# Optimization experiments

Hardware: AMD Instinct MI355X
Metric: run time of the kernel (lower is better)

Reference implementation:

```python
import jax, jax.numpy as jnp
import numpy as np

N = 50000
E = 800000
IN_DIM = 128
OUT_DIM = 128
EDGE_DIM = 3
H = 4
HD = OUT_DIM // H  # 32
SCALE = HD ** -0.5


def setup_inputs() -> dict:
    key = jax.random.key(0)
    ks = jax.random.split(key, 10)
    x = jax.random.normal(ks[0], (N, IN_DIM), dtype=jnp.float32)
    edge_index = jax.random.randint(ks[1], (2, E), 0, N, dtype=jnp.int64)
    edge_attr = jax.random.normal(ks[2], (E, EDGE_DIM), dtype=jnp.float32)
    s = 1.0 / np.sqrt(IN_DIM)
    Wq = jax.random.normal(ks[3], (IN_DIM, H * HD), dtype=jnp.float32) * s
    Wk = jax.random.normal(ks[4], (IN_DIM, H * HD), dtype=jnp.float32) * s
    Wv = jax.random.normal(ks[5], (IN_DIM, H * HD), dtype=jnp.float32) * s
    We = jax.random.normal(ks[6], (EDGE_DIM, H), dtype=jnp.float32) * (1.0 / np.sqrt(EDGE_DIM))
    Wo = jax.random.normal(ks[7], (H * HD, OUT_DIM), dtype=jnp.float32) * (1.0 / np.sqrt(H * HD))
    bo = jnp.zeros((OUT_DIM,), dtype=jnp.float32)
    Wm = jax.random.normal(ks[8], (IN_DIM + OUT_DIM, OUT_DIM), dtype=jnp.float32) * (1.0 / np.sqrt(IN_DIM + OUT_DIM))
    bm = jnp.zeros((OUT_DIM,), dtype=jnp.float32)
    return {"x": x, "edge_index": edge_index, "edge_attr": edge_attr,
            "Wq": Wq, "Wk": Wk, "Wv": Wv, "We": We, "Wo": Wo, "bo": bo,
            "Wm": Wm, "bm": bm}


def reference(x, edge_index, edge_attr, Wq, Wk, Wv, We, Wo, bo, Wm, bm):
    n = x.shape[0]
    src = edge_index[0]
    dst = edge_index[1]
    Q = (x @ Wq).reshape(n, H, HD)
    K = (x @ Wk).reshape(n, H, HD)
    V = (x @ Wv).reshape(n, H, HD)
    edge_bias = edge_attr @ We                                  # [E, H]
    attn = jnp.sum(Q[dst] * K[src], axis=-1) * SCALE + edge_bias  # [E, H]
    attn = jnp.where(attn >= 0, attn, 0.2 * attn)               # leaky_relu(0.2)
    # NOTE: original uses a single GLOBAL max over all edges/heads for stability
    attn_exp = jnp.exp(attn - jnp.max(attn))
    attn_sum = jax.ops.segment_sum(attn_exp, dst, num_segments=n)  # [N, H]
    attn_norm = attn_exp / jnp.maximum(attn_sum[dst], 1e-12)
    # dropout disabled (eval mode)
    weighted_V = V[src] * attn_norm[:, :, None]                 # [E, H, HD]
    agg = jax.ops.segment_sum(weighted_V, dst, num_segments=n)  # [N, H, HD]
    agg = agg.reshape(n, H * HD) @ Wo + bo                      # [N, OUT]
    h = jnp.concatenate([x, agg], axis=1) @ Wm + bm
    return jax.nn.relu(h)
```

## Files before the change

kernel.cpp:

```cpp
#include <hip/hip_runtime.h>
#include <hip/hip_bf16.h>
#include <math.h>

#define NN 50000
#define NE 800000
#define DIM 128
#define NH 4
#define HD 32
#define EH (NE * NH)
#define ATTN_SCALE 0.17677669529663687f
#define MTILE 64
#define GEMM_BLOCKS 782
#define NBKT 98
#define PTS 2048
#define PBLKS 391
#define HBLKS 104

typedef unsigned int uint;
typedef unsigned short ushort;
typedef __attribute__((ext_vector_type(8))) short short8;
typedef __attribute__((ext_vector_type(4))) float f32x4;

__device__ inline ushort f2bf(float f) {
    __hip_bfloat16 h = __float2bfloat16(f);
    return *(ushort*)&h;
}
__device__ inline float bflo(uint u) { return __uint_as_float(u << 16); }
__device__ inline float bfhi(uint u) { return __uint_as_float(u & 0xffff0000u); }

__global__ __launch_bounds__(256) void prep_x_kernel(
    const float* __restrict__ x, ushort* __restrict__ xb)
{
    const int i = blockIdx.x * 256 + threadIdx.x;
    const float4 v = ((const float4*)x)[i];
    ushort4 o;
    o.x = f2bf(v.x); o.y = f2bf(v.y); o.z = f2bf(v.z); o.w = f2bf(v.w);
    ((ushort4*)xb)[i] = o;
}

__global__ __launch_bounds__(128) void prep_wx_kernel(
    const float* __restrict__ Wo, const float* __restrict__ Wm,
    float* __restrict__ Wx)
{
    const int r = blockIdx.x, j = threadIdx.x;
    float acc = 0.f;
    for (int t = 0; t < 128; ++t)
        acc = fmaf(Wo[r * 128 + t], Wm[(128 + t) * 128 + j], acc);
    Wx[r * 128 + j] = acc;
}

__global__ __launch_bounds__(128) void prep_bias_kernel(
    const float* __restrict__ bo, const float* __restrict__ bm,
    const float* __restrict__ Wm, float* __restrict__ bprime)
{
    const int j = threadIdx.x;
    float acc = bm[j];
    for (int t = 0; t < 128; ++t)
        acc = fmaf(bo[t], Wm[(128 + t) * 128 + j], acc);
    bprime[j] = acc;
}

__global__ __launch_bounds__(256) void pack_qkv_kernel(
    const float* __restrict__ Wq, const float* __restrict__ Wk,
    const float* __restrict__ Wv, short* __restrict__ Bp)
{
    const int idx = blockIdx.x * 256 + threadIdx.x;
    const int j = idx & 7, lane = (idx >> 3) & 63;
    const int rest = idx >> 9;
    const int nt = rest % 24, kc = rest / 24;
    const int k = kc * 32 + (lane >> 4) * 8 + j;
    const int n = nt * 16 + (lane & 15);
    const float* W = (n < 128) ? Wq : (n < 256 ? Wk : Wv);
    Bp[idx] = (short)f2bf(W[k * 128 + (n & 127)]);
}

__global__ __launch_bounds__(256) void pack_out_kernel(
    const float* __restrict__ Wm, const float* __restrict__ Wx,
    short* __restrict__ Bp)
{
    const int idx = blockIdx.x * 256 + threadIdx.x;
    const int j = idx & 7, lane = (idx >> 3) & 63;
    const int rest = idx >> 9;
    const int nt = rest & 7, kc = rest >> 3;
    const int k = kc * 32 + (lane >> 4) * 8 + j;
    const int n = nt * 16 + (lane & 15);
    const float v = (k < 128) ? Wm[k * 128 + n] : Wx[(k - 128) * 128 + n];
    Bp[idx] = (short)f2bf(v);
}

__global__ __launch_bounds__(128) void bkt_zero_kernel(int* __restrict__ bkt_cnt)
{
    if (threadIdx.x < 128) bkt_cnt[threadIdx.x] = 0;
}

__global__ __launch_bounds__(256) void bkt_hist_kernel(
    const int* __restrict__ dst, int* __restrict__ bkt_cnt)
{
    __shared__ int c[NBKT];
    const int tid = threadIdx.x;
    if (tid < NBKT) c[tid] = 0;
    __syncthreads();
    for (int e = blockIdx.x * 256 + tid; e < NE; e += HBLKS * 256)
        atomicAdd(&c[dst[e] >> 9], 1);
    __syncthreads();
    if (tid < NBKT && c[tid]) atomicAdd(&bkt_cnt[tid], c[tid]);
}

__global__ void bkt_scan_kernel(const int* __restrict__ bkt_cnt,
                                int* __restrict__ bkt_base,
                                int* __restrict__ bkt_cursor,
                                int* __restrict__ rowptr)
{
    if (threadIdx.x == 0) {
        int run = 0;
        for (int b = 0; b < NBKT; ++b) {
            bkt_base[b] = run;
            bkt_cursor[b] = run;
            run += bkt_cnt[b];
        }
        bkt_base[NBKT] = run;
        rowptr[NN] = run;
    }
}

__global__ __launch_bounds__(256) void partition_kernel(
    const int* __restrict__ src, const int* __restrict__ dst,
    const float* __restrict__ edge_attr, const float* __restrict__ We,
    int* __restrict__ bkt_cursor,
    int* __restrict__ psrc, int* __restrict__ pdst, float* __restrict__ peb)
{
    __shared__ int cnt[NBKT], rbase[NBKT], cnt2[NBKT];
    const int tid = threadIdx.x;
    if (tid < NBKT) cnt[tid] = 0;
    __syncthreads();
    const int e0 = blockIdx.x * PTS;
    #pragma unroll
    for (int it = 0; it < 8; ++it) {
        const int e = e0 + it * 256 + tid;
        if (e < NE) atomicAdd(&cnt[dst[e] >> 9], 1);
    }
    __syncthreads();
    if (tid < NBKT) {
        rbase[tid] = cnt[tid] ? atomicAdd(&bkt_cursor[tid], cnt[tid]) : 0;
        cnt2[tid] = 0;
    }
    __syncthreads();
    #pragma unroll
    for (int it = 0; it < 8; ++it) {
        const int e = e0 + it * 256 + tid;
        if (e < NE) {
            const int d = dst[e];
            const int b = d >> 9;
            const int r = atomicAdd(&cnt2[b], 1);
            const int pos = rbase[b] + r;
            psrc[pos] = src[e];
            pdst[pos] = d;
            const float a0 = edge_attr[e * 3 + 0];
            const float a1 = edge_attr[e * 3 + 1];
            const float a2 = edge_attr[e * 3 + 2];
            float4 eb;
            eb.x = a0 * We[0] + a1 * We[4] + a2 * We[8];
            eb.y = a0 * We[1] + a1 * We[5] + a2 * We[9];
            eb.z = a0 * We[2] + a1 * We[6] + a2 * We[10];
            eb.w = a0 * We[3] + a1 * We[7] + a2 * We[11];
            *(float4*)(peb + (size_t)pos * 4) = eb;
        }
    }
}

__global__ __launch_bounds__(256) void bucket_csr_kernel(
    const int* __restrict__ bkt_base,
    const int* __restrict__ psrc, const int* __restrict__ pdst,
    const float* __restrict__ peb,
    int* __restrict__ rowptr,
    int* __restrict__ srcp, float* __restrict__ eb_csr)
{
    __shared__ int cnt[512];
    __shared__ int pre[512];
    __shared__ int sc[256];
    const int tid = threadIdx.x;
    const int b = blockIdx.x;
    const int base = bkt_base[b];
    const int n = bkt_base[b + 1] - base;
    const int node0 = b << 9;

    cnt[tid] = 0; cnt[tid + 256] = 0;
    __syncthreads();
    for (int i = base + tid; i < base + n; i += 256)
        atomicAdd(&cnt[pdst[i] - node0], 1);
    __syncthreads();

    const int pair = cnt[2 * tid] + cnt[2 * tid + 1];
    sc[tid] = pair;
    __syncthreads();
    for (int off = 1; off < 256; off <<= 1) {
        const int v = (tid >= off) ? sc[tid - off] : 0;
        __syncthreads();
        sc[tid] += v;
        __syncthreads();
    }
    const int ex = sc[tid] - pair;
    pre[2 * tid] = base + ex;
    pre[2 * tid + 1] = base + ex + cnt[2 * tid];
    __syncthreads();

    for (int l = tid; l < 512; l += 256) {
        const int g = node0 + l;
        if (g < NN) rowptr[g] = pre[l];
    }
    __syncthreads();

    for (int i = base + tid; i < base + n; i += 256) {
        const int d = pdst[i];
        const int pos = atomicAdd(&pre[d - node0], 1);
        srcp[pos] = psrc[i];
        *(float4*)(eb_csr + (size_t)pos * 4) =
            *(const float4*)(peb + (size_t)i * 4);
    }
}

__global__ __launch_bounds__(256) void qkv_mfma_kernel(
    const ushort* __restrict__ xb, const short* __restrict__ Bp,
    ushort* __restrict__ Qb, ushort* __restrict__ Kb, ushort* __restrict__ Vb)
{
    const int wave = threadIdx.x >> 6;
    const int lane = threadIdx.x & 63;
    const int m = lane & 15, quad = lane >> 4;
    const int row0w = blockIdx.x * MTILE + wave * 16;
    const int arow = row0w + m;
    const bool rowok = arow < NN;

    short8 a[4];
    #pragma unroll
    for (int kc = 0; kc < 4; ++kc)
        a[kc] = rowok ? *(const short8*)(xb + (size_t)arow * 128 + kc * 32 + quad * 8)
                      : (short8)(0);

    const int NT = 24;
    for (int nt = 0; nt < NT; nt += 2) {
        f32x4 acc0 = {0.f, 0.f, 0.f, 0.f}, acc1 = {0.f, 0.f, 0.f, 0.f};
        #pragma unroll
        for (int kc = 0; kc < 4; ++kc) {
            const short8 b0 = *(const short8*)(Bp + ((size_t)(kc * NT + nt) * 64 + lane) * 8);
            const short8 b1 = *(const short8*)(Bp + ((size_t)(kc * NT + nt + 1) * 64 + lane) * 8);
            acc0 = __builtin_amdgcn_mfma_f32_16x16x32_bf16(a[kc], b0, acc0, 0, 0, 0);
            acc1 = __builtin_amdgcn_mfma_f32_16x16x32_bf16(a[kc], b1, acc1, 0, 0, 0);
        }
        #pragma unroll
        for (int t = 0; t < 2; ++t) {
            const f32x4 acc = t ? acc1 : acc0;
            const int c = (nt + t) * 16 + m;
            ushort* dstp_ = (c < 128) ? Qb : (c < 256 ? Kb : Vb);
            const int lc = c & 127;
            #pragma unroll
            for (int g = 0; g < 4; ++g) {
                const int r = row0w + quad * 4 + g;
                if (r < NN) dstp_[(size_t)r * 128 + lc] = f2bf(acc[g]);
            }
        }
    }
}

__global__ __launch_bounds__(256) void out_mfma_kernel(
    const ushort* __restrict__ xb, const ushort* __restrict__ aggb,
    const short* __restrict__ Bp, const float* __restrict__ bprime,
    float* __restrict__ out)
{
    const int wave = threadIdx.x >> 6;
    const int lane = threadIdx.x & 63;
    const int m = lane & 15, quad = lane >> 4;
    const int row0w = blockIdx.x * MTILE + wave * 16;
    const int arow = row0w + m;
    const bool rowok = arow < NN;

    short8 a[8];
    #pragma unroll
    for (int kc = 0; kc < 4; ++kc)
        a[kc] = rowok ? *(const short8*)(xb + (size_t)arow * 128 + kc * 32 + quad * 8)
                      : (short8)(0);
    #pragma unroll
    for (int kc = 0; kc < 4; ++kc)
        a[4 + kc] = rowok ? *(const short8*)(aggb + (size_t)arow * 128 + kc * 32 + quad * 8)
                          : (short8)(0);

    const int NT = 8;
    for (int nt = 0; nt < NT; nt += 2) {
        f32x4 acc0 = {0.f, 0.f, 0.f, 0.f}, acc1 = {0.f, 0.f, 0.f, 0.f};
        #pragma unroll
        for (int kc = 0; kc < 8; ++kc) {
            const short8 b0 = *(const short8*)(Bp + ((size_t)(kc * NT + nt) * 64 + lane) * 8);
            const short8 b1 = *(const short8*)(Bp + ((size_t)(kc * NT + nt + 1) * 64 + lane) * 8);
            acc0 = __builtin_amdgcn_mfma_f32_16x16x32_bf16(a[kc], b0, acc0, 0, 0, 0);
            acc1 = __builtin_amdgcn_mfma_f32_16x16x32_bf16(a[kc], b1, acc1, 0, 0, 0);
        }
        #pragma unroll
        for (int t = 0; t < 2; ++t) {
            const f32x4 acc = t ? acc1 : acc0;
            const int c = (nt + t) * 16 + m;
            const float bb = bprime[c];
            #pragma unroll
            for (int g = 0; g < 4; ++g) {
                const int r = row0w + quad * 4 + g;
                if (r < NN) out[(size_t)r * 128 + c] = fmaxf(acc[g] + bb, 0.f);
            }
        }
    }
}

__global__ __launch_bounds__(256) void attn_agg_kernel(
    const ushort* __restrict__ Qb, const ushort* __restrict__ Kb,
    const ushort* __restrict__ Vb,
    const int* __restrict__ rowptr, const int* __restrict__ srcp,
    const float* __restrict__ eb_csr, ushort* __restrict__ aggb)
{
    const int tid = threadIdx.x;
    const int d = blockIdx.x * 4 + (tid >> 6);
    const int jj = tid & 63;
    const int h = jj >> 4;
    const int begin = rowptr[d];
    const int end   = rowptr[d + 1];

    const uint uq = *(const uint*)(Qb + (size_t)d * DIM + 2 * jj);
    const float q0 = bflo(uq), q1 = bfhi(uq);

    float ss0 = 0.f, ss1 = 0.f, ss2 = 0.f, ss3 = 0.f;
    float x0 = 0.f, x1 = 0.f, x2 = 0.f, x3 = 0.f;
    float y0 = 0.f, y1 = 0.f, y2 = 0.f, y3 = 0.f;

    int p = begin;
    for (; p + 4 <= end; p += 4) {
        const int s0 = srcp[p + 0];
        const int s1 = srcp[p + 1];
        const int s2 = srcp[p + 2];
        const int s3 = srcp[p + 3];
        const uint k0 = *(const uint*)(Kb + (size_t)s0 * DIM + 2 * jj);
        const uint k1 = *(const uint*)(Kb + (size_t)s1 * DIM + 2 * jj);
        const uint k2 = *(const uint*)(Kb + (size_t)s2 * DIM + 2 * jj);
        const uint k3 = *(const uint*)(Kb + (size_t)s3 * DIM + 2 * jj);
        float p0 = fmaf(q0, bflo(k0), q1 * bfhi(k0));
        float p1 = fmaf(q0, bflo(k1), q1 * bfhi(k1));
        float p2 = fmaf(q0, bflo(k2), q1 * bfhi(k2));
        float p3 = fmaf(q0, bflo(k3), q1 * bfhi(k3));
        #pragma unroll
        for (int m2 = 1; m2 <= 8; m2 <<= 1) {
            p0 += __shfl_xor(p0, m2);
            p1 += __shfl_xor(p1, m2);
            p2 += __shfl_xor(p2, m2);
            p3 += __shfl_xor(p3, m2);
        }
        float a0 = fmaf(p0, ATTN_SCALE, eb_csr[(size_t)(p + 0) * 4 + h]);
        float a1 = fmaf(p1, ATTN_SCALE, eb_csr[(size_t)(p + 1) * 4 + h]);
        float a2 = fmaf(p2, ATTN_SCALE, eb_csr[(size_t)(p + 2) * 4 + h]);
        float a3 = fmaf(p3, ATTN_SCALE, eb_csr[(size_t)(p + 3) * 4 + h]);
        a0 = (a0 >= 0.f) ? a0 : 0.2f * a0;
        a1 = (a1 >= 0.f) ? a1 : 0.2f * a1;
        a2 = (a2 >= 0.f) ? a2 : 0.2f * a2;
        a3 = (a3 >= 0.f) ? a3 : 0.2f * a3;
        const float w0 = __expf(a0);
        const float w1 = __expf(a1);
        const float w2 = __expf(a2);
        const float w3 = __expf(a3);
        const uint v0 = *(const uint*)(Vb + (size_t)s0 * DIM + 2 * jj);
        const uint v1 = *(const uint*)(Vb + (size_t)s1 * DIM + 2 * jj);
        const uint v2 = *(const uint*)(Vb + (size_t)s2 * DIM + 2 * jj);
        const uint v3 = *(const uint*)(Vb + (size_t)s3 * DIM + 2 * jj);
        ss0 += w0; ss1 += w1; ss2 += w2; ss3 += w3;
        x0 = fmaf(w0, bflo(v0), x0); y0 = fmaf(w0, bfhi(v0), y0);
        x1 = fmaf(w1, bflo(v1), x1); y1 = fmaf(w1, bfhi(v1), y1);
        x2 = fmaf(w2, bflo(v2), x2); y2 = fmaf(w2, bfhi(v2), y2);
        x3 = fmaf(w3, bflo(v3), x3); y3 = fmaf(w3, bfhi(v3), y3);
    }
    for (; p < end; ++p) {
        const int s = srcp[p];
        const uint uk = *(const uint*)(Kb + (size_t)s * DIM + 2 * jj);
        float part = fmaf(q0, bflo(uk), q1 * bfhi(uk));
        part += __shfl_xor(part, 1);
        part += __shfl_xor(part, 2);
        part += __shfl_xor(part, 4);
        part += __shfl_xor(part, 8);
        float a = fmaf(part, ATTN_SCALE, eb_csr[(size_t)p * 4 + h]);
        a = (a >= 0.f) ? a : 0.2f * a;
        const float w = __expf(a);
        const uint uv = *(const uint*)(Vb + (size_t)s * DIM + 2 * jj);
        ss0 += w;
        x0 = fmaf(w, bflo(uv), x0);
        y0 = fmaf(w, bfhi(uv), y0);
    }
    const float ssum = (ss0 + ss1) + (ss2 + ss3);
    const float inv = 1.f / fmaxf(ssum, 1e-12f);
    const float ax = ((x0 + x1) + (x2 + x3)) * inv;
    const float ay = ((y0 + y1) + (y2 + y3)) * inv;
    const uint packed = (uint)f2bf(ax) | ((uint)f2bf(ay) << 16);
    *(uint*)(aggb + (size_t)d * DIM + 2 * jj) = packed;
}

extern "C" void kernel_launch(void* const* d_in, const int* in_sizes, int n_in,
                              void* d_out, int out_size, void* d_ws, size_t ws_size,
                              hipStream_t stream)
{
    const float* x         = (const float*)d_in[0];
    const int*   edge_idx  = (const int*)d_in[1];
    const float* edge_attr = (const float*)d_in[2];
    const float* Wq        = (const float*)d_in[3];
    const float* Wk        = (const float*)d_in[4];
    const float* Wv        = (const float*)d_in[5];
    const float* We        = (const float*)d_in[6];
    const float* Wo        = (const float*)d_in[7];
    const float* bo        = (const float*)d_in[8];
    const float* Wm        = (const float*)d_in[9];
    const float* bm        = (const float*)d_in[10];
    float* out = (float*)d_out;

    const int* src = edge_idx;
    const int* dst = edge_idx + NE;

    ushort* xb   = (ushort*)d_ws;
    ushort* Qb   = xb + (size_t)NN * DIM;
    ushort* Kb   = Qb + (size_t)NN * DIM;
    ushort* Vb   = Kb + (size_t)NN * DIM;
    ushort* aggb = Vb + (size_t)NN * DIM;
    int*   psrc     = (int*)(aggb + (size_t)NN * DIM);
    int*   pdst     = psrc + NE;
    float* peb      = (float*)(pdst + NE);
    float* eb_csr   = peb + (size_t)EH;
    float* Wx       = eb_csr + (size_t)EH;
    float* bprime   = Wx + 16384;
    short* BpQKV    = (short*)(bprime + 128);
    short* BpOut    = BpQKV + 49152;
    int*   rowptr   = (int*)(BpOut + 32768);
    int*   srcp     = rowptr + 50048;
    int*   bkt_cnt    = srcp + NE;
    int*   bkt_base   = bkt_cnt + 128;
    int*   bkt_cursor = bkt_base + 128;

    prep_x_kernel<<<(NN * DIM / 4) / 256, 256, 0, stream>>>(x, xb);
    prep_wx_kernel<<<128, 128, 0, stream>>>(Wo, Wm, Wx);
    prep_bias_kernel<<<1, 128, 0, stream>>>(bo, bm, Wm, bprime);
    pack_qkv_kernel<<<192, 256, 0, stream>>>(Wq, Wk, Wv, BpQKV);
    pack_out_kernel<<<128, 256, 0, stream>>>(Wm, Wx, BpOut);

    bkt_zero_kernel<<<1, 128, 0, stream>>>(bkt_cnt);
    bkt_hist_kernel<<<HBLKS, 256, 0, stream>>>(dst, bkt_cnt);
    bkt_scan_kernel<<<1, 64, 0, stream>>>(bkt_cnt, bkt_base, bkt_cursor, rowptr);
    partition_kernel<<<PBLKS, 256, 0, stream>>>(src, dst, edge_attr, We,
                                                bkt_cursor, psrc, pdst, peb);
    bucket_csr_kernel<<<NBKT, 256, 0, stream>>>(bkt_base, psrc, pdst, peb,
                                                rowptr, srcp, eb_csr);

    qkv_mfma_kernel<<<GEMM_BLOCKS, 256, 0, stream>>>(xb, BpQKV, Qb, Kb, Vb);
    attn_agg_kernel<<<NN / 4, 256, 0, stream>>>(Qb, Kb, Vb, rowptr, srcp,
                                                eb_csr, aggb);
    out_mfma_kernel<<<GEMM_BLOCKS, 256, 0, stream>>>(xb, aggb, BpOut, bprime, out);
}
```

Baseline: 295.9 us.

## Interleave K and V rows, store edge bias as bf16, pre-scale src offsets

K and V are written into one interleaved buffer of 256 bf16 per node, so each gathered source node's K and V sit in the same contiguous 512-byte span. This is meant to improve cache and DRAM locality for the random gathers in the attention kernel. Edge bias is packed to bf16 (8 bytes per edge instead of 16), which cuts traffic in partition, CSR build and attention, at some cost in precision. Source indices are stored pre-shifted by 8 so the gather offset needs no multiply, which limits node count to what fits in an int after the shift.

After: 297.0 us. About the same (+0.4%).

```diff
diff --git a/kernel.cpp b/kernel.cpp
--- a/kernel.cpp
+++ b/kernel.cpp
@@ -27,6 +27,7 @@
 }
 __device__ inline float bflo(uint u) { return __uint_as_float(u << 16); }
 __device__ inline float bfhi(uint u) { return __uint_as_float(u & 0xffff0000u); }
+__device__ inline float bfus(ushort u) { return __uint_as_float(((uint)u) << 16); }
 
 __global__ __launch_bounds__(256) void prep_x_kernel(
     const float* __restrict__ x, ushort* __restrict__ xb)
@@ -127,7 +128,7 @@
     const int* __restrict__ src, const int* __restrict__ dst,
     const float* __restrict__ edge_attr, const float* __restrict__ We,
     int* __restrict__ bkt_cursor,
-    int* __restrict__ psrc, int* __restrict__ pdst, float* __restrict__ peb)
+    int* __restrict__ psrc, int* __restrict__ pdst, uint2* __restrict__ peb)
 {
     __shared__ int cnt[NBKT], rbase[NBKT], cnt2[NBKT];
     const int tid = threadIdx.x;
@@ -158,12 +159,14 @@
             const float a0 = edge_attr[e * 3 + 0];
             const float a1 = edge_attr[e * 3 + 1];
             const float a2 = edge_attr[e * 3 + 2];
-            float4 eb;
-            eb.x = a0 * We[0] + a1 * We[4] + a2 * We[8];
-            eb.y = a0 * We[1] + a1 * We[5] + a2 * We[9];
-            eb.z = a0 * We[2] + a1 * We[6] + a2 * We[10];
-            eb.w = a0 * We[3] + a1 * We[7] + a2 * We[11];
-            *(float4*)(peb + (size_t)pos * 4) = eb;
+            const float ex = a0 * We[0] + a1 * We[4] + a2 * We[8];
+            const float ey = a0 * We[1] + a1 * We[5] + a2 * We[9];
+            const float ez = a0 * We[2] + a1 * We[6] + a2 * We[10];
+            const float ew = a0 * We[3] + a1 * We[7] + a2 * We[11];
+            uint2 pk;
+            pk.x = (uint)f2bf(ex) | ((uint)f2bf(ey) << 16);
+            pk.y = (uint)f2bf(ez) | ((uint)f2bf(ew) << 16);
+            peb[pos] = pk;
         }
     }
 }
@@ -171,9 +174,9 @@
 __global__ __launch_bounds__(256) void bucket_csr_kernel(
     const int* __restrict__ bkt_base,
     const int* __restrict__ psrc, const int* __restrict__ pdst,
-    const float* __restrict__ peb,
+    const uint2* __restrict__ peb,
     int* __restrict__ rowptr,
-    int* __restrict__ srcp, float* __restrict__ eb_csr)
+    int* __restrict__ srcp, uint2* __restrict__ eb_csr)
 {
     __shared__ int cnt[512];
     __shared__ int pre[512];
@@ -213,15 +216,14 @@
     for (int i = base + tid; i < base + n; i += 256) {
         const int d = pdst[i];
         const int pos = atomicAdd(&pre[d - node0], 1);
-        srcp[pos] = psrc[i];
-        *(float4*)(eb_csr + (size_t)pos * 4) =
-            *(const float4*)(peb + (size_t)i * 4);
+        srcp[pos] = psrc[i] << 8;
+        eb_csr[pos] = peb[i];
     }
 }
 
 __global__ __launch_bounds__(256) void qkv_mfma_kernel(
     const ushort* __restrict__ xb, const short* __restrict__ Bp,
-    ushort* __restrict__ Qb, ushort* __restrict__ Kb, ushort* __restrict__ Vb)
+    ushort* __restrict__ Qb, ushort* __restrict__ KVb)
 {
     const int wave = threadIdx.x >> 6;
     const int lane = threadIdx.x & 63;
@@ -250,12 +252,13 @@
         for (int t = 0; t < 2; ++t) {
             const f32x4 acc = t ? acc1 : acc0;
             const int c = (nt + t) * 16 + m;
-            ushort* dstp_ = (c < 128) ? Qb : (c < 256 ? Kb : Vb);
-            const int lc = c & 127;
             #pragma unroll
             for (int g = 0; g < 4; ++g) {
                 const int r = row0w + quad * 4 + g;
-                if (r < NN) dstp_[(size_t)r * 128 + lc] = f2bf(acc[g]);
+                if (r < NN) {
+                    if (c < 128) Qb[(size_t)r * 128 + c] = f2bf(acc[g]);
+                    else         KVb[(size_t)r * 256 + (c - 128)] = f2bf(acc[g]);
+                }
             }
         }
     }
@@ -308,10 +311,9 @@
 }
 
 __global__ __launch_bounds__(256) void attn_agg_kernel(
-    const ushort* __restrict__ Qb, const ushort* __restrict__ Kb,
-    const ushort* __restrict__ Vb,
+    const ushort* __restrict__ Qb, const ushort* __restrict__ KVb,
     const int* __restrict__ rowptr, const int* __restrict__ srcp,
-    const float* __restrict__ eb_csr, ushort* __restrict__ aggb)
+    const ushort* __restrict__ ebh, ushort* __restrict__ aggb)
 {
     const int tid = threadIdx.x;
     const int d = blockIdx.x * 4 + (tid >> 6);
@@ -329,14 +331,14 @@
 
     int p = begin;
     for (; p + 4 <= end; p += 4) {
-        const int s0 = srcp[p + 0];
-        const int s1 = srcp[p + 1];
-        const int s2 = srcp[p + 2];
-        const int s3 = srcp[p + 3];
-        const uint k0 = *(const uint*)(Kb + (size_t)s0 * DIM + 2 * jj);
-        const uint k1 = *(const uint*)(Kb + (size_t)s1 * DIM + 2 * jj);
-        const uint k2 = *(const uint*)(Kb + (size_t)s2 * DIM + 2 * jj);
-        const uint k3 = *(const uint*)(Kb + (size_t)s3 * DIM + 2 * jj);
+        const int o0 = srcp[p + 0];
+        const int o1 = srcp[p + 1];
+        const int o2 = srcp[p + 2];
+        const int o3 = srcp[p + 3];
+        const uint k0 = *(const uint*)(KVb + (size_t)o0 + 2 * jj);
+        const uint k1 = *(const uint*)(KVb + (size_t)o1 + 2 * jj);
+        const uint k2 = *(const uint*)(KVb + (size_t)o2 + 2 * jj);
+        const uint k3 = *(const uint*)(KVb + (size_t)o3 + 2 * jj);
         float p0 = fmaf(q0, bflo(k0), q1 * bfhi(k0));
         float p1 = fmaf(q0, bflo(k1), q1 * bfhi(k1));
         float p2 = fmaf(q0, bflo(k2), q1 * bfhi(k2));
@@ -348,10 +350,10 @@
             p2 += __shfl_xor(p2, m2);
             p3 += __shfl_xor(p3, m2);
         }
-        float a0 = fmaf(p0, ATTN_SCALE, eb_csr[(size_t)(p + 0) * 4 + h]);
-        float a1 = fmaf(p1, ATTN_SCALE, eb_csr[(size_t)(p + 1) * 4 + h]);
-        float a2 = fmaf(p2, ATTN_SCALE, eb_csr[(size_t)(p + 2) * 4 + h]);
-        float a3 = fmaf(p3, ATTN_SCALE, eb_csr[(size_t)(p + 3) * 4 + h]);
+        float a0 = fmaf(p0, ATTN_SCALE, bfus(ebh[(size_t)(p + 0) * 4 + h]));
+        float a1 = fmaf(p1, ATTN_SCALE, bfus(ebh[(size_t)(p + 1) * 4 + h]));
+        float a2 = fmaf(p2, ATTN_SCALE, bfus(ebh[(size_t)(p + 2) * 4 + h]));
+        float a3 = fmaf(p3, ATTN_SCALE, bfus(ebh[(size_t)(p + 3) * 4 + h]));
         a0 = (a0 >= 0.f) ? a0 : 0.2f * a0;
         a1 = (a1 >= 0.f) ? a1 : 0.2f * a1;
         a2 = (a2 >= 0.f) ? a2 : 0.2f * a2;
@@ -360,10 +362,10 @@
         const float w1 = __expf(a1);
         const float w2 = __expf(a2);
         const float w3 = __expf(a3);
-        const uint v0 = *(const uint*)(Vb + (size_t)s0 * DIM + 2 * jj);
-        const uint v1 = *(const uint*)(Vb + (size_t)s1 * DIM + 2 * jj);
-        const uint v2 = *(const uint*)(Vb + (size_t)s2 * DIM + 2 * jj);
-        const uint v3 = *(const uint*)(Vb + (size_t)s3 * DIM + 2 * jj);
+        const uint v0 = *(const uint*)(KVb + (size_t)o0 + 128 + 2 * jj);
+        const uint v1 = *(const uint*)(KVb + (size_t)o1 + 128 + 2 * jj);
+        const uint v2 = *(const uint*)(KVb + (size_t)o2 + 128 + 2 * jj);
+        const uint v3 = *(const uint*)(KVb + (size_t)o3 + 128 + 2 * jj);
         ss0 += w0; ss1 += w1; ss2 += w2; ss3 += w3;
         x0 = fmaf(w0, bflo(v0), x0); y0 = fmaf(w0, bfhi(v0), y0);
         x1 = fmaf(w1, bflo(v1), x1); y1 = fmaf(w1, bfhi(v1), y1);
@@ -371,17 +373,17 @@
         x3 = fmaf(w3, bflo(v3), x3); y3 = fmaf(w3, bfhi(v3), y3);
     }
     for (; p < end; ++p) {
-        const int s = srcp[p];
-        const uint uk = *(const uint*)(Kb + (size_t)s * DIM + 2 * jj);
+        const int o = srcp[p];
+        const uint uk = *(const uint*)(KVb + (size_t)o + 2 * jj);
         float part = fmaf(q0, bflo(uk), q1 * bfhi(uk));
         part += __shfl_xor(part, 1);
         part += __shfl_xor(part, 2);
         part += __shfl_xor(part, 4);
         part += __shfl_xor(part, 8);
-        float a = fmaf(part, ATTN_SCALE, eb_csr[(size_t)p * 4 + h]);
+        float a = fmaf(part, ATTN_SCALE, bfus(ebh[(size_t)p * 4 + h]));
         a = (a >= 0.f) ? a : 0.2f * a;
         const float w = __expf(a);
-        const uint uv = *(const uint*)(Vb + (size_t)s * DIM + 2 * jj);
+        const uint uv = *(const uint*)(KVb + (size_t)o + 128 + 2 * jj);
         ss0 += w;
         x0 = fmaf(w, bflo(uv), x0);
         y0 = fmaf(w, bfhi(uv), y0);
@@ -416,14 +418,13 @@
 
     ushort* xb   = (ushort*)d_ws;
     ushort* Qb   = xb + (size_t)NN * DIM;
-    ushort* Kb   = Qb + (size_t)NN * DIM;
-    ushort* Vb   = Kb + (size_t)NN * DIM;
-    ushort* aggb = Vb + (size_t)NN * DIM;
+    ushort* KVb  = Qb + (size_t)NN * DIM;
+    ushort* aggb = KVb + (size_t)NN * 256;
     int*   psrc     = (int*)(aggb + (size_t)NN * DIM);
     int*   pdst     = psrc + NE;
-    float* peb      = (float*)(pdst + NE);
-    float* eb_csr   = peb + (size_t)EH;
-    float* Wx       = eb_csr + (size_t)EH;
+    uint2* peb      = (uint2*)(pdst + NE);
+    uint2* eb_csr   = peb + NE;
+    float* Wx       = (float*)(eb_csr + NE);
     float* bprime   = Wx + 16384;
     short* BpQKV    = (short*)(bprime + 128);
     short* BpOut    = BpQKV + 49152;
@@ -447,8 +448,8 @@
     bucket_csr_kernel<<<NBKT, 256, 0, stream>>>(bkt_base, psrc, pdst, peb,
                                                 rowptr, srcp, eb_csr);
 
-    qkv_mfma_kernel<<<GEMM_BLOCKS, 256, 0, stream>>>(xb, BpQKV, Qb, Kb, Vb);
-    attn_agg_kernel<<<NN / 4, 256, 0, stream>>>(Qb, Kb, Vb, rowptr, srcp,
-                                                eb_csr, aggb);
+    qkv_mfma_kernel<<<GEMM_BLOCKS, 256, 0, stream>>>(xb, BpQKV, Qb, KVb);
+    attn_agg_kernel<<<NN / 4, 256, 0, stream>>>(Qb, KVb, rowptr, srcp,
+                                                (const ushort*)eb_csr, aggb);
     out_mfma_kernel<<<GEMM_BLOCKS, 256, 0, stream>>>(xb, aggb, BpOut, bprime, out);
 }
```
